# Optimization experiments

Hardware: AMD Instinct MI355X
Metric: run time of the kernel (lower is better)

The kernel has to match this reference:

```python
import jax, jax.numpy as jnp
import numpy as np
import math

IMG_CHL = 1024
L_CHL = 512
N_PTS = 4096  # pinned by nn.LayerNorm(4096)
H = 256
W = 256
HEADS = 4
VOXEL = 1.0 / 256.0
PC_MIN = 0.0
BEV_STRIDE = 1.0
LN_EPS = 1e-5


def setup_inputs() -> dict:
    key = jax.random.key(0)
    ks = jax.random.split(key, 6)
    point_features = jax.random.normal(ks[0], (1, L_CHL, N_PTS), jnp.float32)
    kp = jax.random.uniform(ks[1], (N_PTS, 4), dtype=jnp.float32)
    keypoints = kp.at[:, 0].set(0.0)  # batch index column = 0 (batch_size=1)
    bev_features = jax.random.normal(ks[2], (1, IMG_CHL, H, W), jnp.float32)
    conv_L_w = jax.random.normal(ks[3], (L_CHL, L_CHL), jnp.float32) * 0.02
    conv_L_b = jnp.zeros((L_CHL,), jnp.float32)
    img_head_w = jax.random.normal(ks[4], (HEADS, L_CHL, IMG_CHL), jnp.float32) * 0.02
    img_head_b = jnp.zeros((HEADS, L_CHL), jnp.float32)
    ln_w = jnp.ones((N_PTS,), jnp.float32)
    ln_b = jnp.zeros((N_PTS,), jnp.float32)
    conv_fusion_w = jax.random.normal(ks[5], (L_CHL, L_CHL), jnp.float32) * 0.02
    conv_fusion_b = jnp.zeros((L_CHL,), jnp.float32)
    return {
        "point_features": point_features,
        "keypoints": keypoints,
        "bev_features": bev_features,
        "conv_L_w": conv_L_w,
        "conv_L_b": conv_L_b,
        "img_head_w": img_head_w,
        "img_head_b": img_head_b,
        "ln_w": ln_w,
        "ln_b": ln_b,
        "conv_fusion_w": conv_fusion_w,
        "conv_fusion_b": conv_fusion_b,
    }


def _bilinear_interpolate(im, x, y):
    """im: (H, W, C); x, y: (N,). Mirrors bilinear_interpolate_torch (clamped corners)."""
    x0 = jnp.clip(jnp.floor(x).astype(jnp.int32), 0, im.shape[1] - 1)
    x1 = jnp.clip(jnp.floor(x).astype(jnp.int32) + 1, 0, im.shape[1] - 1)
    y0 = jnp.clip(jnp.floor(y).astype(jnp.int32), 0, im.shape[0] - 1)
    y1 = jnp.clip(jnp.floor(y).astype(jnp.int32) + 1, 0, im.shape[0] - 1)
    Ia = im[y0, x0]  # (N, C)
    Ib = im[y1, x0]
    Ic = im[y0, x1]
    Id = im[y1, x1]
    x0f, x1f = x0.astype(x.dtype), x1.astype(x.dtype)
    y0f, y1f = y0.astype(y.dtype), y1.astype(y.dtype)
    wa = (x1f - x) * (y1f - y)
    wb = (x1f - x) * (y - y0f)
    wc = (x - x0f) * (y1f - y)
    wd = (x - x0f) * (y - y0f)
    return Ia * wa[:, None] + Ib * wb[:, None] + Ic * wc[:, None] + Id * wd[:, None]


def reference(point_features, keypoints, bev_features, conv_L_w, conv_L_b,
              img_head_w, img_head_b, ln_w, ln_b, conv_fusion_w, conv_fusion_b):
    # --- interpolate_from_bev_features (batch_size=1, all keypoints in batch 0) ---
    x_idxs = (keypoints[:, 1] - PC_MIN) / VOXEL / BEV_STRIDE
    y_idxs = (keypoints[:, 2] - PC_MIN) / VOXEL / BEV_STRIDE
    im = jnp.transpose(bev_features[0], (1, 2, 0))  # (H, W, C)
    point_bev = _bilinear_interpolate(im, x_idxs, y_idxs)  # (N, IMG_CHL)
    img_features = point_bev.T[None]  # (1, IMG_CHL, N)

    # --- Fusion_Conv_att ---
    # 1x1 Conv1d == channel matmul
    L_query = jnp.einsum('oc,bcn->bon', conv_L_w, point_features) + conv_L_b[None, :, None]  # (1, L, N)
    keys = jnp.einsum('hoc,bcn->hbon', img_head_w, img_features) + img_head_b[:, None, :, None]  # (4, 1, L, N)
    dk = L_CHL
    score = jnp.sum(keys * L_query[None], axis=2)[:, 0, :] / math.sqrt(dk)  # (4, N)
    weightmap = jax.nn.softmax(score, axis=0)[None]  # (1, 4, N) softmax over heads
    z = jnp.einsum('hn,hln->ln', weightmap[0], keys[:, 0])[None]  # (1, L, N)

    t = z + L_query
    mu = jnp.mean(t, axis=-1, keepdims=True)
    var = jnp.mean((t - mu) ** 2, axis=-1, keepdims=True)
    t = (t - mu) / jnp.sqrt(var + LN_EPS) * ln_w + ln_b  # LayerNorm over the 4096 point axis

    fusion_features = jnp.einsum('oc,bcn->bon', conv_fusion_w, t) + conv_fusion_b[None, :, None]
    return fusion_features, weightmap
```

## Files before the change

kernel.cpp:

```cpp
#include <hip/hip_runtime.h>

typedef unsigned short u16;
typedef unsigned int   u32;

typedef short s16x8 __attribute__((ext_vector_type(8)));
typedef float f32x4 __attribute__((ext_vector_type(4)));

__device__ __forceinline__ float b2f(u16 u) {
    u32 x = ((u32)u) << 16;
    float f;
    __builtin_memcpy(&f, &x, 4);
    return f;
}

__device__ __forceinline__ u16 f2b(float f) {
    u32 x;
    __builtin_memcpy(&x, &f, 4);
    u32 r = (x + 0x7fffu + ((x >> 16) & 1u)) >> 16;
    return (u16)r;
}

__device__ __forceinline__ void gload_lds16(const u16* g, u16* l) {
    __builtin_amdgcn_global_load_lds(
        (const __attribute__((address_space(1))) void*)g,
        (__attribute__((address_space(3))) void*)l, 16, 0, 0);
}

__global__ void prep_convert(const float* __restrict__ kp,
                             int4* __restrict__ pts_off,
                             float4* __restrict__ pts_w,
                             int* __restrict__ perm,
                             const float* clw, const float* ihw, const float* cfw,
                             const float* clb, const float* ihb,
                             const float* lnw, const float* lnb, const float* cfb,
                             u16* __restrict__ canon) {
    if (blockIdx.x != 0) {
        const int total = 2632704;
        const int stride = (gridDim.x - 1) * 256;
        for (int i = (blockIdx.x - 1) * 256 + threadIdx.x; i < total; i += stride) {
            const float* src; int off;
            if (i < 262144)       { src = clw; off = i; }
            else if (i < 2359296) { src = ihw; off = i - 262144; }
            else if (i < 2621440) { src = cfw; off = i - 2359296; }
            else if (i < 2621952) { src = clb; off = i - 2621440; }
            else if (i < 2624000) { src = ihb; off = i - 2621952; }
            else if (i < 2628096) { src = lnw; off = i - 2624000; }
            else if (i < 2632192) { src = lnb; off = i - 2628096; }
            else                  { src = cfb; off = i - 2632192; }
            canon[i] = f2b(src[off]);
        }
        return;
    }
    __shared__ int cnt[256];
    __shared__ int base[256];
    const int t = threadIdx.x;
    cnt[t] = 0;
    __syncthreads();
    int buck[16];
    #pragma unroll
    for (int j = 0; j < 16; j++) {
        const int n = j * 256 + t;
        const float x = kp[n * 4 + 1] * 256.0f;
        const float y = kp[n * 4 + 2] * 256.0f;
        const int x0 = min(max((int)floorf(x), 0), 255);
        const int y0 = min(max((int)floorf(y), 0), 255);
        const int b = (y0 >> 3) * 8 + (x0 >> 5);
        buck[j] = b;
        atomicAdd(&cnt[b], 1);
    }
    __syncthreads();
    if (t < 64) {
        int a0 = cnt[t * 4], a1 = cnt[t * 4 + 1], a2 = cnt[t * 4 + 2], a3 = cnt[t * 4 + 3];
        int tot = a0 + a1 + a2 + a3;
        int pre = tot;
        #pragma unroll
        for (int off = 1; off < 64; off <<= 1) {
            int v = __shfl_up(pre, off);
            if (t >= off) pre += v;
        }
        int excl = pre - tot;
        base[t * 4]     = excl;
        base[t * 4 + 1] = excl + a0;
        base[t * 4 + 2] = excl + a0 + a1;
        base[t * 4 + 3] = excl + a0 + a1 + a2;
    }
    __syncthreads();
    cnt[t] = 0;
    __syncthreads();
    #pragma unroll
    for (int j = 0; j < 16; j++) {
        const int n = j * 256 + t;
        const float x = kp[n * 4 + 1] * 256.0f;
        const float y = kp[n * 4 + 2] * 256.0f;
        const float xf = floorf(x), yf = floorf(y);
        const int x0 = min(max((int)xf, 0), 255);
        const int x1 = min(max((int)xf + 1, 0), 255);
        const int y0 = min(max((int)yf, 0), 255);
        const int y1 = min(max((int)yf + 1, 0), 255);
        const float x0f = (float)x0, x1f = (float)x1;
        const float y0f = (float)y0, y1f = (float)y1;
        float4 w;
        w.x = (x1f - x) * (y1f - y);
        w.y = (x1f - x) * (y - y0f);
        w.z = (x - x0f) * (y1f - y);
        w.w = (x - x0f) * (y - y0f);
        int4 o;
        o.x = y0 * 256 + x0;
        o.y = y1 * 256 + x0;
        o.z = y0 * 256 + x1;
        o.w = y1 * 256 + x1;
        const int b = buck[j];
        const int pos = base[b] + atomicAdd(&cnt[b], 1);
        perm[pos] = n;
        pts_off[pos] = o;
        pts_w[pos] = w;
    }
}

__global__ __launch_bounds__(256) void interp_sorted(const float* __restrict__ bev,
                                                     const int4* __restrict__ pts_off,
                                                     const float4* __restrict__ pts_w,
                                                     u16* __restrict__ img) {
    const int c = blockIdx.x;
    const float* plane = bev + (size_t)c * 65536;
    const int base_i = blockIdx.y * 1024;
    const int t = threadIdx.x;
    #pragma unroll
    for (int j = 0; j < 4; j++) {
        const int i = base_i + j * 256 + t;
        const int4 o = pts_off[i];
        const float4 w = pts_w[i];
        const float v = plane[o.x] * w.x + plane[o.y] * w.y +
                        plane[o.z] * w.z + plane[o.w] * w.w;
        img[(size_t)c * 4096 + i] = f2b(v);
    }
}

__global__ void transpose_both(const u16* __restrict__ img, const float* __restrict__ pf,
                               u16* __restrict__ imgT, u16* __restrict__ pfT,
                               const int* __restrict__ perm) {
    __shared__ u16 tile[64][65];
    const int t = threadIdx.x;
    int by = blockIdx.y;
    int isf, R;
    const int* prm;
    u16* out;
    if (by < 16) { isf = 0; R = 1024; prm = perm; out = imgT; }
    else         { isf = 1; R = 512;  prm = nullptr; out = pfT; by -= 16; }
    const int r0 = by * 64, c0 = blockIdx.x * 64;
    #pragma unroll
    for (int i = 0; i < 16; i++) {
        int idx = i * 256 + t;
        int r = idx >> 6, c = idx & 63;
        tile[r][c] = isf ? f2b(pf[(size_t)(r0 + r) * 4096 + c0 + c])
                         : img[(size_t)(r0 + r) * 4096 + c0 + c];
    }
    __syncthreads();
    #pragma unroll
    for (int i = 0; i < 16; i++) {
        int idx = i * 256 + t;
        int c = idx >> 6, r = idx & 63;
        int row = prm ? prm[c0 + c] : (c0 + c);
        out[(size_t)row * R + r0 + r] = tile[r][c];
    }
}

__global__ void transpose_u16(const u16* __restrict__ in, u16* __restrict__ out,
                              int R, int C) {
    __shared__ u16 tile[64][65];
    const int t = threadIdx.x;
    const int r0 = blockIdx.y * 64, c0 = blockIdx.x * 64;
    #pragma unroll
    for (int i = 0; i < 16; i++) {
        int idx = i * 256 + t;
        int r = idx >> 6, c = idx & 63;
        tile[r][c] = in[(size_t)(r0 + r) * C + c0 + c];
    }
    __syncthreads();
    #pragma unroll
    for (int i = 0; i < 16; i++) {
        int idx = i * 256 + t;
        int c = idx >> 6, r = idx & 63;
        out[(size_t)(c0 + c) * R + r0 + r] = tile[r][c];
    }
}

__global__ __launch_bounds__(512, 1) void gemm_k256(const u16* __restrict__ A,
                                                    const u16* __restrict__ BT,
                                                    const u16* __restrict__ bias,
                                                    u16* __restrict__ Cout,
                                                    int M, int N, int K) {
    __shared__ __align__(16) u16 As[4][128 * 32];
    __shared__ __align__(16) u16 Bs[4][256 * 32];
    const int tid = threadIdx.x;
    const int lane = tid & 63;
    const int w = tid >> 6;
    const int bid = blockIdx.x;
    const int swz = (bid & 7) * 32 + (bid >> 3);
    const int m0 = (swz >> 4) * 128;
    const int n0 = (swz & 15) * 256;
    const int wm = (w >> 2) * 64;
    const int wn = (w & 3) * 64;
    const int q = lane >> 4, r = lane & 15;

    const int ra = tid >> 2;
    const int ka = ((tid & 3) ^ (ra & 3)) * 8;
    const int rb0 = tid >> 2;
    const int kb0 = ((tid & 3) ^ (rb0 & 3)) * 8;
    const int sb1 = 512 + tid;
    const int rb1 = sb1 >> 2;
    const int kb1 = ((sb1 & 3) ^ (rb1 & 3)) * 8;

    const int nkt = K >> 5;
    f32x4 acc[4][4] = {};

    {
        gload_lds16(&A[(size_t)(m0 + ra) * K + ka], &As[0][tid * 8]);
        gload_lds16(&BT[(size_t)(n0 + rb0) * K + kb0], &Bs[0][tid * 8]);
        gload_lds16(&BT[(size_t)(n0 + rb1) * K + kb1], &Bs[0][sb1 * 8]);
        gload_lds16(&A[(size_t)(m0 + ra) * K + 32 + ka], &As[1][tid * 8]);
        gload_lds16(&BT[(size_t)(n0 + rb0) * K + 32 + kb0], &Bs[1][tid * 8]);
        gload_lds16(&BT[(size_t)(n0 + rb1) * K + 32 + kb1], &Bs[1][sb1 * 8]);
        asm volatile("s_waitcnt vmcnt(3)" ::: "memory");
        __builtin_amdgcn_s_barrier();
    }

    for (int kt = 0; kt < nkt; kt++) {
        const int b = kt & 3;
        const u16* Ab = As[b];
        const u16* Bb = Bs[b];
        s16x8 af[4], bf[4];
        #pragma unroll
        for (int mt = 0; mt < 4; mt++) {
            const int row = wm + mt * 16 + r;
            af[mt] = *(const s16x8*)&Ab[row * 32 + ((q ^ (row & 3)) * 8)];
        }
        #pragma unroll
        for (int nt = 0; nt < 4; nt++) {
            const int row = wn + nt * 16 + r;
            bf[nt] = *(const s16x8*)&Bb[row * 32 + ((q ^ (row & 3)) * 8)];
        }
        if (kt + 2 < nkt) {
            const int b2 = (kt + 2) & 3;
            const int k2 = (kt + 2) * 32;
            gload_lds16(&A[(size_t)(m0 + ra) * K + k2 + ka], &As[b2][tid * 8]);
            gload_lds16(&BT[(size_t)(n0 + rb0) * K + k2 + kb0], &Bs[b2][tid * 8]);
            gload_lds16(&BT[(size_t)(n0 + rb1) * K + k2 + kb1], &Bs[b2][sb1 * 8]);
        }
        __builtin_amdgcn_s_barrier();
        __builtin_amdgcn_s_setprio(1);
        #pragma unroll
        for (int mt = 0; mt < 4; mt++)
            #pragma unroll
            for (int nt = 0; nt < 4; nt++)
                acc[mt][nt] = __builtin_amdgcn_mfma_f32_16x16x32_bf16(
                    af[mt], bf[nt], acc[mt][nt], 0, 0, 0);
        __builtin_amdgcn_s_setprio(0);
        if (kt + 2 < nkt) asm volatile("s_waitcnt vmcnt(3)" ::: "memory");
        else              asm volatile("s_waitcnt vmcnt(0)" ::: "memory");
        __builtin_amdgcn_s_barrier();
    }

    const int cn = lane & 15;
    #pragma unroll
    for (int mt = 0; mt < 4; mt++) {
        #pragma unroll
        for (int i = 0; i < 4; i++) {
            const int gm = m0 + wm + mt * 16 + q * 4 + i;
            const float bv = b2f(bias[gm]);
            #pragma unroll
            for (int nt = 0; nt < 4; nt++) {
                const int gn = n0 + wn + nt * 16 + cn;
                Cout[(size_t)gm * N + gn] = f2b(acc[mt][nt][i] + bv);
            }
        }
    }
}

template <int BM, int OB>
__global__ __launch_bounds__(256) void gemm_bt(const u16* __restrict__ A,
                                               const u16* __restrict__ BT,
                                               const u16* __restrict__ bias,
                                               void* __restrict__ Cout,
                                               int M, int N, int K) {
    constexpr int MT = BM / 32;
    __shared__ __align__(16) u16 As[BM * 32];
    __shared__ __align__(16) u16 Bs[128 * 32];
    const int tid = threadIdx.x;
    const int lane = tid & 63;
    const int w = tid >> 6;
    const int m0 = blockIdx.y * BM;
    const int n0 = blockIdx.x * 128;
    const int wm = (w >> 1) * (BM / 2);
    const int wn = (w & 1) * 64;

    f32x4 acc[MT][4] = {};

    const int q = lane >> 4, r = lane & 15;

    for (int k0 = 0; k0 < K; k0 += 32) {
        __syncthreads();
        #pragma unroll
        for (int i = 0; i < BM / 64; i++) {
            int s = i * 256 + tid;
            gload_lds16(&A[(size_t)(m0 + (s >> 2)) * K + k0 + (s & 3) * 8], &As[s * 8]);
        }
        #pragma unroll
        for (int i = 0; i < 2; i++) {
            int s = i * 256 + tid;
            gload_lds16(&BT[(size_t)(n0 + (s >> 2)) * K + k0 + (s & 3) * 8], &Bs[s * 8]);
        }
        __syncthreads();

        s16x8 af[MT], bfr[4];
        #pragma unroll
        for (int mt = 0; mt < MT; mt++)
            af[mt] = *(const s16x8*)&As[(wm + mt * 16 + r) * 32 + q * 8];
        #pragma unroll
        for (int nt = 0; nt < 4; nt++)
            bfr[nt] = *(const s16x8*)&Bs[(wn + nt * 16 + r) * 32 + q * 8];
        #pragma unroll
        for (int mt = 0; mt < MT; mt++)
            #pragma unroll
            for (int nt = 0; nt < 4; nt++)
                acc[mt][nt] = __builtin_amdgcn_mfma_f32_16x16x32_bf16(
                    af[mt], bfr[nt], acc[mt][nt], 0, 0, 0);
    }

    const int cn = lane & 15;
    #pragma unroll
    for (int mt = 0; mt < MT; mt++) {
        #pragma unroll
        for (int i = 0; i < 4; i++) {
            int gm = m0 + wm + mt * 16 + q * 4 + i;
            float bv = b2f(bias[gm]);
            #pragma unroll
            for (int nt = 0; nt < 4; nt++) {
                int gn = n0 + wn + nt * 16 + cn;
                float v = acc[mt][nt][i] + bv;
                if (OB)
                    ((u16*)Cout)[(size_t)gm * N + gn] = f2b(v);
                else
                    ((float*)Cout)[(size_t)gm * N + gn] = v;
            }
        }
    }
}

__global__ __launch_bounds__(512) void score_softmax(const u16* __restrict__ keys,
                                                     const float* __restrict__ lq,
                                                     float* __restrict__ wm_ws,
                                                     float* __restrict__ out) {
    __shared__ float red[4][8][64];
    const int nl = threadIdx.x & 63;
    const int ls = threadIdx.x >> 6;
    const int n = blockIdx.x * 64 + nl;
    float acc[4] = {0.f, 0.f, 0.f, 0.f};
    #pragma unroll 8
    for (int i = 0; i < 64; i++) {
        const int l = ls * 64 + i;
        const float qv = lq[l * 4096 + n];
        #pragma unroll
        for (int h = 0; h < 4; h++)
            acc[h] += b2f(keys[(size_t)(h * 512 + l) * 4096 + n]) * qv;
    }
    #pragma unroll
    for (int h = 0; h < 4; h++) red[h][ls][nl] = acc[h];
    __syncthreads();
    if (threadIdx.x < 64) {
        const float scale = 0.044194173824159216f;
        float s[4];
        #pragma unroll
        for (int h = 0; h < 4; h++) {
            float v = 0.f;
            #pragma unroll
            for (int c = 0; c < 8; c++) v += red[h][c][nl];
            s[h] = v * scale;
        }
        float mx = fmaxf(fmaxf(s[0], s[1]), fmaxf(s[2], s[3]));
        float e[4], sum = 0.f;
        #pragma unroll
        for (int h = 0; h < 4; h++) { e[h] = expf(s[h] - mx); sum += e[h]; }
        const float inv = 1.0f / sum;
        #pragma unroll
        for (int h = 0; h < 4; h++) {
            float wv = e[h] * inv;
            wm_ws[h * 4096 + n] = wv;
            out[2097152 + (size_t)h * 4096 + n] = wv;
        }
    }
}

__global__ __launch_bounds__(256) void compute_t_ln(const u16* __restrict__ keys,
                                                    const float* __restrict__ lq,
                                                    const float* __restrict__ wm_ws,
                                                    const float* __restrict__ lnw,
                                                    const float* __restrict__ lnb,
                                                    u16* __restrict__ tnorm) {
    const int l = blockIdx.x;
    const int t = threadIdx.x;
    float tv[16];
    float s = 0.f, ss = 0.f;
    #pragma unroll
    for (int j = 0; j < 16; j++) {
        const int n = j * 256 + t;
        float v = lq[l * 4096 + n];
        #pragma unroll
        for (int h = 0; h < 4; h++)
            v += wm_ws[h * 4096 + n] * b2f(keys[(size_t)(h * 512 + l) * 4096 + n]);
        tv[j] = v;
        s += v;
        ss += v * v;
    }
    for (int off = 32; off > 0; off >>= 1) {
        s += __shfl_down(s, off);
        ss += __shfl_down(ss, off);
    }
    __shared__ float bs[4], bss[4];
    const int w = t >> 6, lane = t & 63;
    if (lane == 0) { bs[w] = s; bss[w] = ss; }
    __syncthreads();
    const float S = bs[0] + bs[1] + bs[2] + bs[3];
    const float SS = bss[0] + bss[1] + bss[2] + bss[3];
    const float mu = S * (1.0f / 4096.0f);
    const float rstd = rsqrtf(SS * (1.0f / 4096.0f) - mu * mu + 1e-5f);
    #pragma unroll
    for (int j = 0; j < 16; j++) {
        const int n = j * 256 + t;
        const float v = (tv[j] - mu) * rstd * lnw[n] + lnb[n];
        tnorm[(size_t)l * 4096 + n] = f2b(v);
    }
}

extern "C" void kernel_launch(void* const* d_in, const int* in_sizes, int n_in,
                              void* d_out, int out_size, void* d_ws, size_t ws_size,
                              hipStream_t stream) {
    const float* pf  = (const float*)d_in[0];
    const float* kp  = (const float*)d_in[1];
    const float* bev = (const float*)d_in[2];
    const float* clw = (const float*)d_in[3];
    const float* clb = (const float*)d_in[4];
    const float* ihw = (const float*)d_in[5];
    const float* ihb = (const float*)d_in[6];
    const float* lnw = (const float*)d_in[7];
    const float* lnb = (const float*)d_in[8];
    const float* cfw = (const float*)d_in[9];
    const float* cfb = (const float*)d_in[10];
    float* out = (float*)d_out;

    char* ws = (char*)d_ws;
    u16*    img     = (u16*)(ws + 0);
    u16*    tnorm   = (u16*)(ws + 0);
    u16*    imgT    = (u16*)(ws + (8ull << 20));
    float*  lq      = (float*)(ws + (8ull << 20));
    u16*    keys    = (u16*)(ws + (16ull << 20));
    u16*    pfT     = (u16*)(ws + (32ull << 20));
    u16*    tT      = (u16*)(ws + (32ull << 20));
    float*  wm_ws   = (float*)(ws + (36ull << 20));
    u16*    canon   = (u16*)  (ws + (36ull << 20) + 131072);
    int4*   pts_off = (int4*) (ws + (42ull << 20));
    float4* pts_w   = (float4*)(ws + (42ull << 20) + 65536);
    int*    perm    = (int*)  (ws + (42ull << 20) + 131072);

    u16* clw_c = canon;
    u16* ihw_c = canon + 262144;
    u16* cfw_c = canon + 2359296;
    u16* clb_c = canon + 2621440;
    u16* ihb_c = canon + 2621952;
    u16* cfb_c = canon + 2632192;

    prep_convert<<<1025, 256, 0, stream>>>(kp, pts_off, pts_w, perm,
                                           clw, ihw, cfw, clb, ihb, lnw, lnb, cfb, canon);
    interp_sorted<<<dim3(1024, 4), 256, 0, stream>>>(bev, pts_off, pts_w, img);
    transpose_both<<<dim3(64, 24), 256, 0, stream>>>(img, pf, imgT, pfT, perm);
    gemm_k256<<<256, 512, 0, stream>>>(ihw_c, imgT, ihb_c, keys, 2048, 4096, 1024);
    gemm_bt<64, 0><<<dim3(32, 8), 256, 0, stream>>>(clw_c, pfT, clb_c, lq, 512, 4096, 512);
    score_softmax<<<64, 512, 0, stream>>>(keys, lq, wm_ws, out);
    compute_t_ln<<<512, 256, 0, stream>>>(keys, lq, wm_ws, lnw, lnb, tnorm);
    transpose_u16<<<dim3(64, 8), 256, 0, stream>>>(tnorm, tT, 512, 4096);
    gemm_bt<64, 0><<<dim3(32, 8), 256, 0, stream>>>(cfw_c, tT, cfb_c, out, 512, 4096, 512);
}
```

Baseline: 491.5 us.

## Fuse t computation into score kernel, fuse LN with transpose, deepen GEMM K-tile

The score kernel now also computes t = lq + sum_h w_h*keys while keys and lq are hot, writing fp32 t plus per-block partial sum and sum-of-squares. A new kernel reduces those partials and applies LayerNorm while transposing, replacing the separate compute_t_ln and transpose launches and their reread of keys. The main keys GEMM also moves from K-tile 32 with 4 stages to K-tile 64 with 3 stages and an 8-wide XOR swizzle. The trade-off is an fp32 intermediate buffer, only 64 blocks doing the extra t work, and more LDS in the GEMM.

```diff
diff --git a/kernel.cpp b/kernel.cpp
--- a/kernel.cpp
+++ b/kernel.cpp
@@ -165,33 +165,13 @@
     }
 }
 
-__global__ void transpose_u16(const u16* __restrict__ in, u16* __restrict__ out,
-                              int R, int C) {
-    __shared__ u16 tile[64][65];
-    const int t = threadIdx.x;
-    const int r0 = blockIdx.y * 64, c0 = blockIdx.x * 64;
-    #pragma unroll
-    for (int i = 0; i < 16; i++) {
-        int idx = i * 256 + t;
-        int r = idx >> 6, c = idx & 63;
-        tile[r][c] = in[(size_t)(r0 + r) * C + c0 + c];
-    }
-    __syncthreads();
-    #pragma unroll
-    for (int i = 0; i < 16; i++) {
-        int idx = i * 256 + t;
-        int c = idx >> 6, r = idx & 63;
-        out[(size_t)(c0 + c) * R + r0 + r] = tile[r][c];
-    }
-}
-
 __global__ __launch_bounds__(512, 1) void gemm_k256(const u16* __restrict__ A,
                                                     const u16* __restrict__ BT,
                                                     const u16* __restrict__ bias,
                                                     u16* __restrict__ Cout,
                                                     int M, int N, int K) {
-    __shared__ __align__(16) u16 As[4][128 * 32];
-    __shared__ __align__(16) u16 Bs[4][256 * 32];
+    __shared__ __align__(16) u16 As[3][128 * 64];
+    __shared__ __align__(16) u16 Bs[3][256 * 64];
     const int tid = threadIdx.x;
     const int lane = tid & 63;
     const int w = tid >> 6;
@@ -203,60 +183,78 @@
     const int wn = (w & 3) * 64;
     const int q = lane >> 4, r = lane & 15;
 
-    const int ra = tid >> 2;
-    const int ka = ((tid & 3) ^ (ra & 3)) * 8;
-    const int rb0 = tid >> 2;
-    const int kb0 = ((tid & 3) ^ (rb0 & 3)) * 8;
-    const int sb1 = 512 + tid;
-    const int rb1 = sb1 >> 2;
-    const int kb1 = ((sb1 & 3) ^ (rb1 & 3)) * 8;
-
-    const int nkt = K >> 5;
+    int ra[2], ca[2];
+    #pragma unroll
+    for (int i = 0; i < 2; i++) {
+        int s = i * 512 + tid;
+        ra[i] = s >> 3;
+        ca[i] = ((s & 7) ^ (ra[i] & 7)) * 8;
+    }
+    int rb[4], cb[4];
+    #pragma unroll
+    for (int i = 0; i < 4; i++) {
+        int s = i * 512 + tid;
+        rb[i] = s >> 3;
+        cb[i] = ((s & 7) ^ (rb[i] & 7)) * 8;
+    }
+
+    const int nkt = K >> 6;
     f32x4 acc[4][4] = {};
 
-    {
-        gload_lds16(&A[(size_t)(m0 + ra) * K + ka], &As[0][tid * 8]);
-        gload_lds16(&BT[(size_t)(n0 + rb0) * K + kb0], &Bs[0][tid * 8]);
-        gload_lds16(&BT[(size_t)(n0 + rb1) * K + kb1], &Bs[0][sb1 * 8]);
-        gload_lds16(&A[(size_t)(m0 + ra) * K + 32 + ka], &As[1][tid * 8]);
-        gload_lds16(&BT[(size_t)(n0 + rb0) * K + 32 + kb0], &Bs[1][tid * 8]);
-        gload_lds16(&BT[(size_t)(n0 + rb1) * K + 32 + kb1], &Bs[1][sb1 * 8]);
-        asm volatile("s_waitcnt vmcnt(3)" ::: "memory");
-        __builtin_amdgcn_s_barrier();
-    }
+    #pragma unroll
+    for (int tkt = 0; tkt < 2; tkt++) {
+        const int kb = tkt * 64;
+        #pragma unroll
+        for (int i = 0; i < 2; i++)
+            gload_lds16(&A[(size_t)(m0 + ra[i]) * K + kb + ca[i]], &As[tkt][(i * 512 + tid) * 8]);
+        #pragma unroll
+        for (int i = 0; i < 4; i++)
+            gload_lds16(&BT[(size_t)(n0 + rb[i]) * K + kb + cb[i]], &Bs[tkt][(i * 512 + tid) * 8]);
+    }
+    asm volatile("s_waitcnt vmcnt(6)" ::: "memory");
+    __builtin_amdgcn_s_barrier();
 
     for (int kt = 0; kt < nkt; kt++) {
-        const int b = kt & 3;
-        const u16* Ab = As[b];
-        const u16* Bb = Bs[b];
-        s16x8 af[4], bf[4];
+        const int sl = kt % 3;
+        const u16* Ab = As[sl];
+        const u16* Bb = Bs[sl];
+        s16x8 af[4][2], bf[4][2];
         #pragma unroll
         for (int mt = 0; mt < 4; mt++) {
             const int row = wm + mt * 16 + r;
-            af[mt] = *(const s16x8*)&Ab[row * 32 + ((q ^ (row & 3)) * 8)];
+            #pragma unroll
+            for (int kh = 0; kh < 2; kh++)
+                af[mt][kh] = *(const s16x8*)&Ab[row * 64 + (((kh * 4 + q) ^ (r & 7)) * 8)];
         }
         #pragma unroll
         for (int nt = 0; nt < 4; nt++) {
             const int row = wn + nt * 16 + r;
-            bf[nt] = *(const s16x8*)&Bb[row * 32 + ((q ^ (row & 3)) * 8)];
+            #pragma unroll
+            for (int kh = 0; kh < 2; kh++)
+                bf[nt][kh] = *(const s16x8*)&Bb[row * 64 + (((kh * 4 + q) ^ (r & 7)) * 8)];
         }
         if (kt + 2 < nkt) {
-            const int b2 = (kt + 2) & 3;
-            const int k2 = (kt + 2) * 32;
-            gload_lds16(&A[(size_t)(m0 + ra) * K + k2 + ka], &As[b2][tid * 8]);
-            gload_lds16(&BT[(size_t)(n0 + rb0) * K + k2 + kb0], &Bs[b2][tid * 8]);
-            gload_lds16(&BT[(size_t)(n0 + rb1) * K + k2 + kb1], &Bs[b2][sb1 * 8]);
+            const int s2 = (kt + 2) % 3;
+            const int kb = (kt + 2) * 64;
+            #pragma unroll
+            for (int i = 0; i < 2; i++)
+                gload_lds16(&A[(size_t)(m0 + ra[i]) * K + kb + ca[i]], &As[s2][(i * 512 + tid) * 8]);
+            #pragma unroll
+            for (int i = 0; i < 4; i++)
+                gload_lds16(&BT[(size_t)(n0 + rb[i]) * K + kb + cb[i]], &Bs[s2][(i * 512 + tid) * 8]);
         }
         __builtin_amdgcn_s_barrier();
         __builtin_amdgcn_s_setprio(1);
         #pragma unroll
-        for (int mt = 0; mt < 4; mt++)
-            #pragma unroll
-            for (int nt = 0; nt < 4; nt++)
-                acc[mt][nt] = __builtin_amdgcn_mfma_f32_16x16x32_bf16(
-                    af[mt], bf[nt], acc[mt][nt], 0, 0, 0);
+        for (int kh = 0; kh < 2; kh++)
+            #pragma unroll
+            for (int mt = 0; mt < 4; mt++)
+                #pragma unroll
+                for (int nt = 0; nt < 4; nt++)
+                    acc[mt][nt] = __builtin_amdgcn_mfma_f32_16x16x32_bf16(
+                        af[mt][kh], bf[nt][kh], acc[mt][nt], 0, 0, 0);
         __builtin_amdgcn_s_setprio(0);
-        if (kt + 2 < nkt) asm volatile("s_waitcnt vmcnt(3)" ::: "memory");
+        if (kt + 2 < nkt) asm volatile("s_waitcnt vmcnt(6)" ::: "memory");
         else              asm volatile("s_waitcnt vmcnt(0)" ::: "memory");
         __builtin_amdgcn_s_barrier();
     }
@@ -347,25 +345,28 @@
     }
 }
 
-__global__ __launch_bounds__(512) void score_softmax(const u16* __restrict__ keys,
-                                                     const float* __restrict__ lq,
-                                                     float* __restrict__ wm_ws,
-                                                     float* __restrict__ out) {
+__global__ __launch_bounds__(512) void score_t(const u16* __restrict__ keys,
+                                               const float* __restrict__ lq,
+                                               float* __restrict__ wm_ws,
+                                               float* __restrict__ out,
+                                               float* __restrict__ tbuf,
+                                               float* __restrict__ stat_part) {
     __shared__ float red[4][8][64];
+    __shared__ float wm_sh[4][64];
     const int nl = threadIdx.x & 63;
-    const int ls = threadIdx.x >> 6;
+    const int lg = threadIdx.x >> 6;
     const int n = blockIdx.x * 64 + nl;
     float acc[4] = {0.f, 0.f, 0.f, 0.f};
     #pragma unroll 8
     for (int i = 0; i < 64; i++) {
-        const int l = ls * 64 + i;
+        const int l = lg * 64 + i;
         const float qv = lq[l * 4096 + n];
         #pragma unroll
         for (int h = 0; h < 4; h++)
             acc[h] += b2f(keys[(size_t)(h * 512 + l) * 4096 + n]) * qv;
     }
     #pragma unroll
-    for (int h = 0; h < 4; h++) red[h][ls][nl] = acc[h];
+    for (int h = 0; h < 4; h++) red[h][lg][nl] = acc[h];
     __syncthreads();
     if (threadIdx.x < 64) {
         const float scale = 0.044194173824159216f;
@@ -385,50 +386,72 @@
         #pragma unroll
         for (int h = 0; h < 4; h++) {
             float wv = e[h] * inv;
+            wm_sh[h][nl] = wv;
             wm_ws[h * 4096 + n] = wv;
             out[2097152 + (size_t)h * 4096 + n] = wv;
         }
     }
-}
-
-__global__ __launch_bounds__(256) void compute_t_ln(const u16* __restrict__ keys,
-                                                    const float* __restrict__ lq,
-                                                    const float* __restrict__ wm_ws,
-                                                    const float* __restrict__ lnw,
-                                                    const float* __restrict__ lnb,
-                                                    u16* __restrict__ tnorm) {
-    const int l = blockIdx.x;
+    __syncthreads();
+    float wv[4];
+    #pragma unroll
+    for (int h = 0; h < 4; h++) wv[h] = wm_sh[h][nl];
+    const int sbase = blockIdx.x * 1024;
+    for (int j = 0; j < 64; j++) {
+        const int l = lg * 64 + j;
+        float v = lq[l * 4096 + n];
+        #pragma unroll
+        for (int h = 0; h < 4; h++)
+            v += wv[h] * b2f(keys[(size_t)(h * 512 + l) * 4096 + n]);
+        tbuf[(size_t)l * 4096 + n] = v;
+        float s = v, ss = v * v;
+        #pragma unroll
+        for (int off = 32; off > 0; off >>= 1) {
+            s += __shfl_down(s, off);
+            ss += __shfl_down(ss, off);
+        }
+        if (nl == 0) {
+            stat_part[sbase + l] = s;
+            stat_part[sbase + 512 + l] = ss;
+        }
+    }
+}
+
+__global__ __launch_bounds__(256) void tnorm_transpose(const float* __restrict__ tbuf,
+                                                       const float* __restrict__ stat_part,
+                                                       const float* __restrict__ lnw,
+                                                       const float* __restrict__ lnb,
+                                                       u16* __restrict__ tT) {
+    __shared__ u16 tile[64][65];
+    __shared__ float smu[64], srs[64], slw[64], slb[64];
     const int t = threadIdx.x;
-    float tv[16];
-    float s = 0.f, ss = 0.f;
-    #pragma unroll
-    for (int j = 0; j < 16; j++) {
-        const int n = j * 256 + t;
-        float v = lq[l * 4096 + n];
-        #pragma unroll
-        for (int h = 0; h < 4; h++)
-            v += wm_ws[h * 4096 + n] * b2f(keys[(size_t)(h * 512 + l) * 4096 + n]);
-        tv[j] = v;
-        s += v;
-        ss += v * v;
-    }
-    for (int off = 32; off > 0; off >>= 1) {
-        s += __shfl_down(s, off);
-        ss += __shfl_down(ss, off);
-    }
-    __shared__ float bs[4], bss[4];
-    const int w = t >> 6, lane = t & 63;
-    if (lane == 0) { bs[w] = s; bss[w] = ss; }
-    __syncthreads();
-    const float S = bs[0] + bs[1] + bs[2] + bs[3];
-    const float SS = bss[0] + bss[1] + bss[2] + bss[3];
-    const float mu = S * (1.0f / 4096.0f);
-    const float rstd = rsqrtf(SS * (1.0f / 4096.0f) - mu * mu + 1e-5f);
-    #pragma unroll
-    for (int j = 0; j < 16; j++) {
-        const int n = j * 256 + t;
-        const float v = (tv[j] - mu) * rstd * lnw[n] + lnb[n];
-        tnorm[(size_t)l * 4096 + n] = f2b(v);
+    const int l0 = blockIdx.y * 64, n0 = blockIdx.x * 64;
+    if (t < 64) {
+        float s = 0.f, ss = 0.f;
+        #pragma unroll 8
+        for (int b = 0; b < 64; b++) {
+            s  += stat_part[b * 1024 + l0 + t];
+            ss += stat_part[b * 1024 + 512 + l0 + t];
+        }
+        const float mu = s * (1.0f / 4096.0f);
+        smu[t] = mu;
+        srs[t] = rsqrtf(ss * (1.0f / 4096.0f) - mu * mu + 1e-5f);
+        slw[t] = lnw[n0 + t];
+        slb[t] = lnb[n0 + t];
+    }
+    __syncthreads();
+    #pragma unroll
+    for (int i = 0; i < 16; i++) {
+        int idx = i * 256 + t;
+        int r = idx >> 6, c = idx & 63;
+        const float v = (tbuf[(size_t)(l0 + r) * 4096 + n0 + c] - smu[r]) * srs[r] * slw[c] + slb[c];
+        tile[r][c] = f2b(v);
+    }
+    __syncthreads();
+    #pragma unroll
+    for (int i = 0; i < 16; i++) {
+        int idx = i * 256 + t;
+        int c = idx >> 6, r = idx & 63;
+        tT[(size_t)(n0 + c) * 512 + l0 + r] = tile[r][c];
     }
 }
 
@@ -450,7 +473,7 @@
 
     char* ws = (char*)d_ws;
     u16*    img     = (u16*)(ws + 0);
-    u16*    tnorm   = (u16*)(ws + 0);
+    float*  tbuf    = (float*)(ws + 0);
     u16*    imgT    = (u16*)(ws + (8ull << 20));
     float*  lq      = (float*)(ws + (8ull << 20));
     u16*    keys    = (u16*)(ws + (16ull << 20));
@@ -461,6 +484,7 @@
     int4*   pts_off = (int4*) (ws + (42ull << 20));
     float4* pts_w   = (float4*)(ws + (42ull << 20) + 65536);
     int*    perm    = (int*)  (ws + (42ull << 20) + 131072);
+    float*  stat_p  = (float*)(ws + (43ull << 20));
 
     u16* clw_c = canon;
     u16* ihw_c = canon + 262144;
@@ -475,8 +499,7 @@
     transpose_both<<<dim3(64, 24), 256, 0, stream>>>(img, pf, imgT, pfT, perm);
     gemm_k256<<<256, 512, 0, stream>>>(ihw_c, imgT, ihb_c, keys, 2048, 4096, 1024);
     gemm_bt<64, 0><<<dim3(32, 8), 256, 0, stream>>>(clw_c, pfT, clb_c, lq, 512, 4096, 512);
-    score_softmax<<<64, 512, 0, stream>>>(keys, lq, wm_ws, out);
-    compute_t_ln<<<512, 256, 0, stream>>>(keys, lq, wm_ws, lnw, lnb, tnorm);
-    transpose_u16<<<dim3(64, 8), 256, 0, stream>>>(tnorm, tT, 512, 4096);
+    score_t<<<64, 512, 0, stream>>>(keys, lq, wm_ws, out, tbuf, stat_p);
+    tnorm_transpose<<<dim3(64, 8), 256, 0, stream>>>(tbuf, stat_p, lnw, lnb, tT);
     gemm_bt<64, 0><<<dim3(32, 8), 256, 0, stream>>>(cfw_c, tT, cfb_c, out, 512, 4096, 512);
 }
```

After: 523.6 us. 6.5% more time.
